# Kernel tuning notes

Measured on AMD Instinct MI355X. Metric: run time of the kernel, lower is better.

Reference implementation:

```python
import jax, jax.numpy as jnp
import numpy as np

D_MODEL = 1024
NUM_HEADS = 16
D_K = D_MODEL // NUM_HEADS
ROPE_THETA = 10000.0


def apply_rope(x, pos):
    # x: [B, H, S, d_k], pos: [S] int
    half = x.shape[-1] // 2
    inv_freq = ROPE_THETA ** (-jnp.arange(half, dtype=jnp.float32) * 2.0 / x.shape[-1])
    ang = pos.astype(jnp.float32)[:, None] * inv_freq[None, :]  # [S, half]
    cos, sin = jnp.cos(ang), jnp.sin(ang)
    x1 = x[..., 0::2]
    x2 = x[..., 1::2]
    r1 = x1 * cos - x2 * sin
    r2 = x1 * sin + x2 * cos
    return jnp.stack([r1, r2], axis=-1).reshape(x.shape)


def setup_inputs() -> dict:
    key = jax.random.key(0)
    ks = jax.random.split(key, 5)
    B, S = 4, 2048
    scale = 1.0 / np.sqrt(D_MODEL)
    x = jax.random.normal(ks[0], (B, S, D_MODEL), dtype=jnp.float32)
    w_q = jax.random.normal(ks[1], (D_MODEL, D_MODEL), dtype=jnp.float32) * scale
    w_k = jax.random.normal(ks[2], (D_MODEL, D_MODEL), dtype=jnp.float32) * scale
    w_v = jax.random.normal(ks[3], (D_MODEL, D_MODEL), dtype=jnp.float32) * scale
    w_o = jax.random.normal(ks[4], (D_MODEL, D_MODEL), dtype=jnp.float32) * scale
    token_positions = jnp.arange(S, dtype=jnp.int32)
    return {"x": x, "w_q": w_q, "w_k": w_k, "w_v": w_v, "w_o": w_o, "token_positions": token_positions}


def reference(x, w_q, w_k, w_v, w_o, token_positions):
    B, S, _ = x.shape
    def proj(w):
        return (x @ w.T).reshape(B, S, NUM_HEADS, D_K).transpose(0, 2, 1, 3)  # [B,H,S,d_k]
    q, k, v = proj(w_q), proj(w_k), proj(w_v)
    q = apply_rope(q, token_positions)
    k = apply_rope(k, token_positions)
    logits = jnp.einsum('bhid,bhjd->bhij', q, k) / jnp.sqrt(jnp.float32(D_K))
    causal = jnp.tril(jnp.ones((S, S), dtype=bool))
    logits = jnp.where(causal[None, None], logits, -jnp.inf)
    weights = jax.nn.softmax(logits, axis=-1)
    attn = jnp.einsum('bhij,bhjd->bhid', weights, v)  # [B,H,S,d_k]
    attn = attn.transpose(0, 2, 1, 3).reshape(B, S, D_MODEL)
    return attn @ w_o.T
```

## Files before the change

### kernel.cpp

```cpp
#include <hip/hip_runtime.h>
#include <hip/hip_bf16.h>
#include <stdint.h>

#define DM   1024
#define SEQ  2048
#define BATCH 4
#define NH   16
#define DK   64
#define NTK  16

typedef __attribute__((ext_vector_type(8))) __bf16 bf16x8;
typedef __attribute__((ext_vector_type(4))) float f32x4;
typedef __attribute__((ext_vector_type(4))) unsigned short ushort4_t;
typedef __attribute__((ext_vector_type(4))) unsigned int uint4_t;

typedef __attribute__((address_space(1))) const unsigned int GU32;
typedef __attribute__((address_space(3))) unsigned int LU32;

__device__ inline void gl_lds16(const void* g, void* l) {
  __builtin_amdgcn_global_load_lds((GU32*)g, (LU32*)l, 16, 0, 0);
}

__device__ inline f32x4 mfma16(bf16x8 a, bf16x8 b, f32x4 c) {
  return __builtin_amdgcn_mfma_f32_16x16x32_bf16(a, b, c, 0, 0, 0);
}

__device__ inline unsigned short f2bf(float f) {
  unsigned u = __float_as_uint(f);
  u += 0x7fffu + ((u >> 16) & 1u);
  return (unsigned short)(u >> 16);
}

__device__ inline unsigned cvt_pk_bf16(float a, float b) {
  unsigned r;
  asm("v_cvt_pk_bf16_f32 %0, %1, %2" : "=v"(r) : "v"(a), "v"(b));
  return r;
}

__device__ inline float fexp2(float x) {
  float r;
  asm("v_exp_f32 %0, %1" : "=v"(r) : "v"(x));
  return r;
}

__device__ inline float fmax3(float a, float b, float c) {
  float r;
  asm("v_max3_f32 %0, %1, %2, %3" : "=v"(r) : "v"(a), "v"(b), "v"(c));
  return r;
}

__device__ inline int swz_of(int r) { return ((r & 6) << 2) | ((r & 1) << 5); }
__device__ inline int bswz(int r) { return ((r & 6) << 3) | ((r & 1) << 6); }

__global__ void prep_kernel(const float* __restrict__ x,
                            const float* __restrict__ wq, const float* __restrict__ wk,
                            const float* __restrict__ wv, const float* __restrict__ wo,
                            const int* __restrict__ tp,
                            unsigned short* __restrict__ xbf,
                            unsigned short* __restrict__ wbf,
                            float2* __restrict__ tab)
{
  const int NX4 = (BATCH*SEQ*DM)/4;
  const int NW4 = (DM*DM)/4;
  int idx = blockIdx.x*256 + threadIdx.x;
  if (idx < NX4) {
    float4 v = ((const float4*)x)[idx];
    ushort4_t o; o[0]=f2bf(v.x); o[1]=f2bf(v.y); o[2]=f2bf(v.z); o[3]=f2bf(v.w);
    ((ushort4_t*)xbf)[idx] = o;
  } else if (idx < NX4 + 4*NW4) {
    int t = idx - NX4;
    int wsel = t >> 18;
    int off = t & (NW4-1);
    const float* src = (wsel==0) ? wq : (wsel==1) ? wk : (wsel==2) ? wv : wo;
    float4 v = ((const float4*)src)[off];
    ushort4_t o; o[0]=f2bf(v.x); o[1]=f2bf(v.y); o[2]=f2bf(v.z); o[3]=f2bf(v.w);
    ((ushort4_t*)wbf)[wsel*NW4 + off] = o;
  } else {
    int t = idx - NX4 - 4*NW4;
    if (t < SEQ*32) {
      int s = t >> 5, i = t & 31;
      float invf = exp2f(-(float)i * (13.287712379549449f/32.0f));
      float ang = (float)tp[s] * invf;
      float sn, cs; sincosf(ang, &sn, &cs);
      tab[t] = make_float2(cs, sn);
    }
  }
}

template<int MODE>
__global__ __launch_bounds__(256, 2)
void gemm_db(const unsigned short* __restrict__ A,
             const unsigned short* __restrict__ Wall,
             unsigned short* __restrict__ qbf,
             unsigned short* __restrict__ kbf,
             unsigned short* __restrict__ vt,
             float* __restrict__ ofp,
             const float2* __restrict__ tab)
{
  __shared__ __align__(16) char lds[65536];
  const int tid = threadIdx.x;
  const int bid = blockIdx.x;
  int sel, mt, nt;
  if (MODE == 0) {
    sel = bid >> 9;
    int r = bid & 511;
    int xcd = r & 7, idx = r >> 3;
    mt = xcd*8 + (idx >> 3);  nt = idx & 7;
  } else {
    sel = 3;
    int xcd = bid & 7, idx = bid >> 3;
    mt = xcd*8 + (idx >> 3);  nt = idx & 7;
  }
  const unsigned short* Bm = Wall + (size_t)sel*DM*DM;
  const int a0 = mt*128, b0r = nt*128;
  const int w = tid>>6, lane = tid&63, ln = lane&15, g = lane>>4;
  const int wm = (w>>1)*64, wn = (w&1)*64;

  const char* src[8];
  {
    int rr = tid >> 3;
    int c  = (tid & 7) * 8;
    #pragma unroll
    for (int i = 0; i < 4; ++i) {
      int r_ = i*32 + rr;
      int cs = c ^ swz_of(r_);
      src[i]   = (const char*)(A  + (size_t)(a0  + r_)*DM + cs);
      src[i+4] = (const char*)(Bm + (size_t)(b0r + r_)*DM + cs);
    }
  }

  int offA[4], offB[4];
  #pragma unroll
  for (int m = 0; m < 4; ++m) {
    int R  = wm + m*16 + ln;
    offA[m] = R*128 + ((g*8 ^ swz_of(R)) * 2);
    int Rb = wn + m*16 + ln;
    offB[m] = 16384 + Rb*128 + ((g*8 ^ swz_of(Rb)) * 2);
  }

  f32x4 acc[4][4];
  #pragma unroll
  for (int i=0;i<4;i++)
    #pragma unroll
    for (int j=0;j<4;j++) acc[i][j] = (f32x4){0.f,0.f,0.f,0.f};

  #pragma unroll
  for (int i = 0; i < 8; ++i) gl_lds16(src[i],       lds +         i*4096 + tid*16);
  #pragma unroll
  for (int i = 0; i < 8; ++i) gl_lds16(src[i] + 128, lds + 32768 + i*4096 + tid*16);

  for (int t = 0; t < NTK; ++t) {
    char* sb = lds + (t & 1) * 32768;
    if (t < NTK-1) asm volatile("s_waitcnt vmcnt(8)" ::: "memory");
    else           asm volatile("s_waitcnt vmcnt(0)" ::: "memory");
    __builtin_amdgcn_sched_barrier(0);
    __builtin_amdgcn_s_barrier();
    asm volatile("" ::: "memory");
    __builtin_amdgcn_sched_barrier(0);

    bf16x8 fa[4][2], fb[4][2];
    #pragma unroll
    for (int m = 0; m < 4; ++m) {
      fa[m][0] = *(const bf16x8*)(sb + offA[m]);
      fa[m][1] = *(const bf16x8*)(sb + (offA[m] ^ 64));
      fb[m][0] = *(const bf16x8*)(sb + offB[m]);
      fb[m][1] = *(const bf16x8*)(sb + (offB[m] ^ 64));
    }
    asm volatile("s_waitcnt lgkmcnt(0)" ::: "memory");
    __builtin_amdgcn_sched_barrier(0);
    __builtin_amdgcn_s_barrier();
    asm volatile("" ::: "memory");
    __builtin_amdgcn_sched_barrier(0);

    if (t + 2 < NTK) {
      const int kb = (t + 2) * 128;
      #pragma unroll
      for (int i = 0; i < 8; ++i)
        gl_lds16(src[i] + kb, sb + i*4096 + tid*16);
    }
    __builtin_amdgcn_s_setprio(1);
    #pragma unroll
    for (int h = 0; h < 2; ++h)
      #pragma unroll
      for (int m = 0; m < 4; ++m)
        #pragma unroll
        for (int n = 0; n < 4; ++n)
          acc[m][n] = mfma16(fa[m][h], fb[n][h], acc[m][n]);
    __builtin_amdgcn_s_setprio(0);
  }

  if (MODE == 1) {
    #pragma unroll
    for (int i=0;i<4;i++) {
      int m = a0 + wm + i*16 + g*4;
      #pragma unroll
      for (int jn=0;jn<4;jn++) {
        int n = b0r + wn + jn*16 + ln;
        #pragma unroll
        for (int j=0;j<4;j++)
          ofp[(size_t)(m+j)*DM + n] = acc[i][jn][j];
      }
    }
  } else if (sel == 2) {
    #pragma unroll
    for (int i=0;i<4;i++) {
      int m0 = a0 + wm + i*16 + g*4;
      int bb = m0>>11, s0 = m0&2047;
      #pragma unroll
      for (int jn=0;jn<4;jn++) {
        int n = b0r + wn + jn*16 + ln;
        int h = n>>6, d = n&63;
        ushort4_t o4;
        #pragma unroll
        for (int j=0;j<4;j++) o4[j] = f2bf(acc[i][jn][j]);
        *(ushort4_t*)&vt[(((size_t)bb*NH + h)*DK + d)*SEQ + s0] = o4;
      }
    }
  } else {
    unsigned short* dst = sel ? kbf : qbf;
    const float qs = sel ? 1.0f : 0.1803368802f;
    #pragma unroll
    for (int jn=0;jn<4;jn++) {
      int n = b0r + wn + jn*16 + ln;
      int h = n>>6, d = n&63, di = d>>1, par = d&1;
      #pragma unroll
      for (int i=0;i<4;i++) {
        #pragma unroll
        for (int j=0;j<4;j++) {
          int m = a0 + wm + i*16 + g*4 + j;
          int bb = m>>11, s = m&2047;
          float v = acc[i][jn][j];
          float pv = __shfl_xor(v, 1);
          float2 cssn = tab[s*32 + di];
          float r = par ? (v*cssn.x + pv*cssn.y) : (v*cssn.x - pv*cssn.y);
          dst[((size_t)(bb*NH + h)*SEQ + s)*DK + d] = f2bf(r*qs);
        }
      }
    }
  }
}

__global__ __launch_bounds__(256, 2)
void attn_fa(const unsigned short* __restrict__ qbf,
             const unsigned short* __restrict__ kbf,
             const unsigned short* __restrict__ vtg,
             unsigned short* __restrict__ attnbf)
{
  __shared__ __align__(16) char kv_lds[32768];
  __shared__ unsigned short PlA[4][16][72];
  __shared__ unsigned short PlB[4][16][72];
  const int bh = blockIdx.x, qblk = 15 - blockIdx.y;
  const int tid = threadIdx.x, w = tid>>6, lane = tid&63, ln = lane&15, g = lane>>4;
  const int q0a = qblk*128 + w*16;
  const int q0b = q0a + 64;
  const int NT = 2*qblk + 2;

  const unsigned short* qrowA = qbf + ((size_t)bh*SEQ + q0a + ln)*DK;
  const unsigned short* qrowB = qbf + ((size_t)bh*SEQ + q0b + ln)*DK;
  bf16x8 qa0 = *(const bf16x8*)(qrowA + g*8);
  bf16x8 qa1 = *(const bf16x8*)(qrowA + 32 + g*8);
  bf16x8 qb0 = *(const bf16x8*)(qrowB + g*8);
  bf16x8 qb1 = *(const bf16x8*)(qrowB + 32 + g*8);

  uint4_t ov = {0x3F803F80u, 0x3F803F80u, 0x3F803F80u, 0x3F803F80u};
  const bf16x8 ones = *(bf16x8*)&ov;

  const int rr = tid >> 3;
  const int cb = (tid & 7) * 16;
  const char* ks0 = (const char*)(kbf + ((size_t)bh*SEQ + rr     )*DK) + (cb ^ bswz(rr));
  const char* ks1 = (const char*)(kbf + ((size_t)bh*SEQ + rr + 32)*DK) + (cb ^ bswz(rr));
  const char* vs0 = (const char*)(vtg + ((size_t)bh*DK  + rr     )*SEQ) + (cb ^ bswz(rr));
  const char* vs1 = (const char*)(vtg + ((size_t)bh*DK  + rr + 32)*SEQ) + (cb ^ bswz(rr));

  const int ok0 = (g*16) ^ bswz(ln);

  gl_lds16(ks0, kv_lds +         tid*16);
  gl_lds16(ks1, kv_lds +  4096 + tid*16);
  gl_lds16(vs0, kv_lds +  8192 + tid*16);
  gl_lds16(vs1, kv_lds + 12288 + tid*16);
  gl_lds16(ks0 + 8192, kv_lds + 16384 +         tid*16);
  gl_lds16(ks1 + 8192, kv_lds + 16384 +  4096 + tid*16);
  gl_lds16(vs0 + 128,  kv_lds + 16384 +  8192 + tid*16);
  gl_lds16(vs1 + 128,  kv_lds + 16384 + 12288 + tid*16);

  f32x4 oA[4], oB[4], osA, osB;
  #pragma unroll
  for (int f=0;f<4;f++) { oA[f] = (f32x4){0,0,0,0}; oB[f] = (f32x4){0,0,0,0}; }
  osA = (f32x4){0,0,0,0}; osB = (f32x4){0,0,0,0};
  float mA = -1e30f, mB = -1e30f;
  const int qgA = q0a + ln, qgB = q0b + ln;

  for (int t = 0; t < NT; ++t) {
    char* sb = kv_lds + (t & 1) * 16384;
    if (t < NT-1) asm volatile("s_waitcnt vmcnt(4)" ::: "memory");
    else          asm volatile("s_waitcnt vmcnt(0)" ::: "memory");
    __builtin_amdgcn_sched_barrier(0);
    __builtin_amdgcn_s_barrier();
    asm volatile("" ::: "memory");
    __builtin_amdgcn_sched_barrier(0);

    bf16x8 kf[4][2], vfr[4][2];
    #pragma unroll
    for (int a=0;a<4;a++) {
      kf[a][0]  = *(const bf16x8*)(sb + a*2048 + (ok0 ^  0) + ln*128);
      kf[a][1]  = *(const bf16x8*)(sb + a*2048 + (ok0 ^ 64) + ln*128);
      vfr[a][0] = *(const bf16x8*)(sb + 8192 + a*2048 + (ok0 ^  0) + ln*128);
      vfr[a][1] = *(const bf16x8*)(sb + 8192 + a*2048 + (ok0 ^ 64) + ln*128);
    }
    asm volatile("s_waitcnt lgkmcnt(0)" ::: "memory");
    __builtin_amdgcn_sched_barrier(0);
    __builtin_amdgcn_s_barrier();
    asm volatile("" ::: "memory");
    __builtin_amdgcn_sched_barrier(0);

    if (t + 2 < NT) {
      const size_t kO = (size_t)(t+2)*8192, vO = (size_t)(t+2)*128;
      gl_lds16(ks0 + kO, sb +         tid*16);
      gl_lds16(ks1 + kO, sb +  4096 + tid*16);
      gl_lds16(vs0 + vO, sb +  8192 + tid*16);
      gl_lds16(vs1 + vO, sb + 12288 + tid*16);
    }

    const bool actA = (t < NT-1);

    f32x4 saA[4], saB[4];
    __builtin_amdgcn_s_setprio(1);
    #pragma unroll
    for (int kvf=0;kvf<4;kvf++) {
      f32x4 zb = (f32x4){0,0,0,0};
      zb = mfma16(kf[kvf][0], qb0, zb);
      zb = mfma16(kf[kvf][1], qb1, zb);
      saB[kvf] = zb;
    }
    if (actA) {
      #pragma unroll
      for (int kvf=0;kvf<4;kvf++) {
        f32x4 za = (f32x4){0,0,0,0};
        za = mfma16(kf[kvf][0], qa0, za);
        za = mfma16(kf[kvf][1], qa1, za);
        saA[kvf] = za;
      }
    }
    __builtin_amdgcn_s_setprio(0);

    if (actA) {
      if (t == NT-2) {
        int thr = qgA - t*64 - g*4;
        #pragma unroll
        for (int kvf=0;kvf<4;kvf++)
          #pragma unroll
          for (int j=0;j<4;j++)
            if (kvf*16 + j > thr) saA[kvf][j] = -1e30f;
      }
      float lm = fmax3(saA[0][0], saA[0][1], saA[0][2]);
      lm = fmax3(lm, saA[0][3], saA[1][0]);
      lm = fmax3(lm, saA[1][1], saA[1][2]);
      lm = fmax3(lm, saA[1][3], saA[2][0]);
      lm = fmax3(lm, saA[2][1], saA[2][2]);
      lm = fmax3(lm, saA[2][3], saA[3][0]);
      lm = fmax3(lm, saA[3][1], saA[3][2]);
      lm = fmaxf(lm, saA[3][3]);
      lm = fmaxf(lm, __shfl_xor(lm, 16));
      lm = fmaxf(lm, __shfl_xor(lm, 32));
      if (!__all(lm - mA <= 8.0f)) {
        float mnew = fmaxf(mA, lm);
        float corr = fexp2(mA - mnew);
        #pragma unroll
        for (int j=0;j<4;j++) {
          float cj = __shfl(corr, g*4 + j);
          #pragma unroll
          for (int f=0;f<4;f++) oA[f][j] *= cj;
          osA[j] *= cj;
        }
        mA = mnew;
      }
      #pragma unroll
      for (int kvf=0;kvf<4;kvf++) {
        float p0 = fexp2(saA[kvf][0] - mA);
        float p1 = fexp2(saA[kvf][1] - mA);
        float p2 = fexp2(saA[kvf][2] - mA);
        float p3 = fexp2(saA[kvf][3] - mA);
        uint2 pk;
        pk.x = cvt_pk_bf16(p0, p1);
        pk.y = cvt_pk_bf16(p2, p3);
        *(uint2*)&PlA[w][ln][kvf*16 + g*4] = pk;
      }
    }

    {
      if (t == NT-1) {
        int thr = qgB - t*64 - g*4;
        #pragma unroll
        for (int kvf=0;kvf<4;kvf++)
          #pragma unroll
          for (int j=0;j<4;j++)
            if (kvf*16 + j > thr) saB[kvf][j] = -1e30f;
      }
      float lm = fmax3(saB[0][0], saB[0][1], saB[0][2]);
      lm = fmax3(lm, saB[0][3], saB[1][0]);
      lm = fmax3(lm, saB[1][1], saB[1][2]);
      lm = fmax3(lm, saB[1][3], saB[2][0]);
      lm = fmax3(lm, saB[2][1], saB[2][2]);
      lm = fmax3(lm, saB[2][3], saB[3][0]);
      lm = fmax3(lm, saB[3][1], saB[3][2]);
      lm = fmaxf(lm, saB[3][3]);
      lm = fmaxf(lm, __shfl_xor(lm, 16));
      lm = fmaxf(lm, __shfl_xor(lm, 32));
      if (!__all(lm - mB <= 8.0f)) {
        float mnew = fmaxf(mB, lm);
        float corr = fexp2(mB - mnew);
        #pragma unroll
        for (int j=0;j<4;j++) {
          float cj = __shfl(corr, g*4 + j);
          #pragma unroll
          for (int f=0;f<4;f++) oB[f][j] *= cj;
          osB[j] *= cj;
        }
        mB = mnew;
      }
      #pragma unroll
      for (int kvf=0;kvf<4;kvf++) {
        float p0 = fexp2(saB[kvf][0] - mB);
        float p1 = fexp2(saB[kvf][1] - mB);
        float p2 = fexp2(saB[kvf][2] - mB);
        float p3 = fexp2(saB[kvf][3] - mB);
        uint2 pk;
        pk.x = cvt_pk_bf16(p0, p1);
        pk.y = cvt_pk_bf16(p2, p3);
        *(uint2*)&PlB[w][ln][kvf*16 + g*4] = pk;
      }
    }

    asm volatile("s_waitcnt lgkmcnt(0)" ::: "memory");

    __builtin_amdgcn_s_setprio(1);
    #pragma unroll
    for (int c=0;c<2;c++) {
      bf16x8 pfB = *(const bf16x8*)&PlB[w][ln][c*32 + g*8];
      #pragma unroll
      for (int f=0;f<4;f++)
        oB[f] = mfma16(pfB, vfr[f][c], oB[f]);
      osB = mfma16(pfB, ones, osB);
    }
    if (actA) {
      #pragma unroll
      for (int c=0;c<2;c++) {
        bf16x8 pfA = *(const bf16x8*)&PlA[w][ln][c*32 + g*8];
        #pragma unroll
        for (int f=0;f<4;f++)
          oA[f] = mfma16(pfA, vfr[f][c], oA[f]);
        osA = mfma16(pfA, ones, osA);
      }
    }
    __builtin_amdgcn_s_setprio(0);
  }

  const int bb = bh>>4, h = bh&15;
  #pragma unroll
  for (int j=0;j<4;j++) {
    float liA = 1.0f / osA[j];
    float liB = 1.0f / osB[j];
    int sA = q0a + g*4 + j, sB = q0b + g*4 + j;
    #pragma unroll
    for (int f=0;f<4;f++) {
      attnbf[((size_t)bb*SEQ + sA)*DM + h*DK + f*16 + ln] = f2bf(oA[f][j]*liA);
      attnbf[((size_t)bb*SEQ + sB)*DM + h*DK + f*16 + ln] = f2bf(oB[f][j]*liB);
    }
  }
}

extern "C" void kernel_launch(void* const* d_in, const int* in_sizes, int n_in,
                              void* d_out, int out_size, void* d_ws, size_t ws_size,
                              hipStream_t stream)
{
  const float* x  = (const float*)d_in[0];
  const float* wq = (const float*)d_in[1];
  const float* wk = (const float*)d_in[2];
  const float* wv = (const float*)d_in[3];
  const float* wo = (const float*)d_in[4];
  const int*   tp = (const int*)d_in[5];

  const size_t XB = (size_t)BATCH*SEQ*DM*2;
  const size_t WB = (size_t)DM*DM*2;

  char* ws = (char*)d_ws;
  unsigned short* xbf = (unsigned short*)(ws);
  unsigned short* qbf = (unsigned short*)(ws + XB);
  unsigned short* kbf = (unsigned short*)(ws + 2*XB);
  unsigned short* vt  = (unsigned short*)(ws + 3*XB);
  unsigned short* abf = (unsigned short*)(ws + 4*XB);
  unsigned short* wbf = (unsigned short*)(ws + 5*XB);
  float2* tab = (float2*)(ws + 5*XB + 4*WB);

  prep_kernel<<<12544, 256, 0, stream>>>(x, wq, wk, wv, wo, tp, xbf, wbf, tab);

  gemm_db<0><<<1536, 256, 0, stream>>>(xbf, wbf, qbf, kbf, vt, nullptr, tab);
  attn_fa<<<dim3(64,16), 256, 0, stream>>>(qbf, kbf, vt, abf);
  gemm_db<1><<<512, 256, 0, stream>>>(abf, wbf, nullptr, nullptr, nullptr,
                                      (float*)d_out, nullptr);
}
```

Baseline: 176.0 us.

## Pair complementary causal query blocks per workgroup to balance attention work

Each attention workgroup now handles two query blocks, qh=15-by and by, processing their KV tiles back to back in one continuous double-buffered loop of 34 tiles. The grid is halved to 64x8. Every block gets the same causal workload, which removes tail imbalance and lets the KV prefetch pipeline run across the boundary between the two query blocks. The trade-off is fewer workgroups, which reduces occupancy slack. It also adds a mid-loop epilogue that writes the first block's output and reloads Q.

```diff
diff --git a/kernel.cpp b/kernel.cpp
--- a/kernel.cpp
+++ b/kernel.cpp
@@ -249,18 +249,12 @@
   __shared__ __align__(16) char kv_lds[32768];
   __shared__ unsigned short PlA[4][16][72];
   __shared__ unsigned short PlB[4][16][72];
-  const int bh = blockIdx.x, qblk = 15 - blockIdx.y;
+  const int bh = blockIdx.x, by = blockIdx.y;
+  const int qh = 15 - by;
+  const int NTa = 2*qh + 2;
+  const int NTtot = 34;
   const int tid = threadIdx.x, w = tid>>6, lane = tid&63, ln = lane&15, g = lane>>4;
-  const int q0a = qblk*128 + w*16;
-  const int q0b = q0a + 64;
-  const int NT = 2*qblk + 2;
-
-  const unsigned short* qrowA = qbf + ((size_t)bh*SEQ + q0a + ln)*DK;
-  const unsigned short* qrowB = qbf + ((size_t)bh*SEQ + q0b + ln)*DK;
-  bf16x8 qa0 = *(const bf16x8*)(qrowA + g*8);
-  bf16x8 qa1 = *(const bf16x8*)(qrowA + 32 + g*8);
-  bf16x8 qb0 = *(const bf16x8*)(qrowB + g*8);
-  bf16x8 qb1 = *(const bf16x8*)(qrowB + 32 + g*8);
+  const int bb = bh>>4, h = bh&15;
 
   uint4_t ov = {0x3F803F80u, 0x3F803F80u, 0x3F803F80u, 0x3F803F80u};
   const bf16x8 ones = *(bf16x8*)&ov;
@@ -283,17 +277,27 @@
   gl_lds16(vs0 + 128,  kv_lds + 16384 +  8192 + tid*16);
   gl_lds16(vs1 + 128,  kv_lds + 16384 + 12288 + tid*16);
 
+  int q0a = qh*128 + w*16;
+  int q0b = q0a + 64;
+  const unsigned short* qrowA = qbf + ((size_t)bh*SEQ + q0a + ln)*DK;
+  const unsigned short* qrowB = qbf + ((size_t)bh*SEQ + q0b + ln)*DK;
+  bf16x8 qa0 = *(const bf16x8*)(qrowA + g*8);
+  bf16x8 qa1 = *(const bf16x8*)(qrowA + 32 + g*8);
+  bf16x8 qb0 = *(const bf16x8*)(qrowB + g*8);
+  bf16x8 qb1 = *(const bf16x8*)(qrowB + 32 + g*8);
+
   f32x4 oA[4], oB[4], osA, osB;
   #pragma unroll
   for (int f=0;f<4;f++) { oA[f] = (f32x4){0,0,0,0}; oB[f] = (f32x4){0,0,0,0}; }
   osA = (f32x4){0,0,0,0}; osB = (f32x4){0,0,0,0};
   float mA = -1e30f, mB = -1e30f;
-  const int qgA = q0a + ln, qgB = q0b + ln;
-
-  for (int t = 0; t < NT; ++t) {
-    char* sb = kv_lds + (t & 1) * 16384;
-    if (t < NT-1) asm volatile("s_waitcnt vmcnt(4)" ::: "memory");
-    else          asm volatile("s_waitcnt vmcnt(0)" ::: "memory");
+
+  for (int u = 0; u < NTtot; ++u) {
+    const int tloc  = (u < NTa) ? u : u - NTa;
+    const int NTcur = (u < NTa) ? NTa : NTtot - NTa;
+    char* sb = kv_lds + (u & 1) * 16384;
+    if (u < NTtot-1) asm volatile("s_waitcnt vmcnt(4)" ::: "memory");
+    else             asm volatile("s_waitcnt vmcnt(0)" ::: "memory");
     __builtin_amdgcn_sched_barrier(0);
     __builtin_amdgcn_s_barrier();
     asm volatile("" ::: "memory");
@@ -313,15 +317,42 @@
     asm volatile("" ::: "memory");
     __builtin_amdgcn_sched_barrier(0);
 
-    if (t + 2 < NT) {
-      const size_t kO = (size_t)(t+2)*8192, vO = (size_t)(t+2)*128;
+    if (u + 2 < NTtot) {
+      const int t2 = (u + 2 < NTa) ? u + 2 : u + 2 - NTa;
+      const size_t kO = (size_t)t2*8192, vO = (size_t)t2*128;
       gl_lds16(ks0 + kO, sb +         tid*16);
       gl_lds16(ks1 + kO, sb +  4096 + tid*16);
       gl_lds16(vs0 + vO, sb +  8192 + tid*16);
       gl_lds16(vs1 + vO, sb + 12288 + tid*16);
     }
 
-    const bool actA = (t < NT-1);
+    if (u == NTa) {
+      #pragma unroll
+      for (int j=0;j<4;j++) {
+        float liA = 1.0f / osA[j];
+        float liB = 1.0f / osB[j];
+        int sA = q0a + g*4 + j, sB = q0b + g*4 + j;
+        #pragma unroll
+        for (int f=0;f<4;f++) {
+          attnbf[((size_t)bb*SEQ + sA)*DM + h*DK + f*16 + ln] = f2bf(oA[f][j]*liA);
+          attnbf[((size_t)bb*SEQ + sB)*DM + h*DK + f*16 + ln] = f2bf(oB[f][j]*liB);
+        }
+      }
+      q0a = by*128 + w*16;
+      q0b = q0a + 64;
+      const unsigned short* qrA = qbf + ((size_t)bh*SEQ + q0a + ln)*DK;
+      const unsigned short* qrB = qbf + ((size_t)bh*SEQ + q0b + ln)*DK;
+      qa0 = *(const bf16x8*)(qrA + g*8);
+      qa1 = *(const bf16x8*)(qrA + 32 + g*8);
+      qb0 = *(const bf16x8*)(qrB + g*8);
+      qb1 = *(const bf16x8*)(qrB + 32 + g*8);
+      #pragma unroll
+      for (int f=0;f<4;f++) { oA[f] = (f32x4){0,0,0,0}; oB[f] = (f32x4){0,0,0,0}; }
+      osA = (f32x4){0,0,0,0}; osB = (f32x4){0,0,0,0};
+      mA = -1e30f; mB = -1e30f;
+    }
+
+    const bool actA = (tloc < NTcur-1);
 
     f32x4 saA[4], saB[4];
     __builtin_amdgcn_s_setprio(1);
@@ -344,8 +375,8 @@
     __builtin_amdgcn_s_setprio(0);
 
     if (actA) {
-      if (t == NT-2) {
-        int thr = qgA - t*64 - g*4;
+      if (tloc == NTcur-2) {
+        int thr = q0a + ln - tloc*64 - g*4;
         #pragma unroll
         for (int kvf=0;kvf<4;kvf++)
           #pragma unroll
@@ -388,8 +419,8 @@
     }
 
     {
-      if (t == NT-1) {
-        int thr = qgB - t*64 - g*4;
+      if (tloc == NTcur-1) {
+        int thr = q0b + ln - tloc*64 - g*4;
         #pragma unroll
         for (int kvf=0;kvf<4;kvf++)
           #pragma unroll
@@ -455,7 +486,6 @@
     __builtin_amdgcn_s_setprio(0);
   }
 
-  const int bb = bh>>4, h = bh&15;
   #pragma unroll
   for (int j=0;j<4;j++) {
     float liA = 1.0f / osA[j];
@@ -495,7 +525,7 @@
   prep_kernel<<<12544, 256, 0, stream>>>(x, wq, wk, wv, wo, tp, xbf, wbf, tab);
 
   gemm_db<0><<<1536, 256, 0, stream>>>(xbf, wbf, qbf, kbf, vt, nullptr, tab);
-  attn_fa<<<dim3(64,16), 256, 0, stream>>>(qbf, kbf, vt, abf);
+  attn_fa<<<dim3(64,8), 256, 0, stream>>>(qbf, kbf, vt, abf);
   gemm_db<1><<<512, 256, 0, stream>>>(abf, wbf, nullptr, nullptr, nullptr,
                                       (float*)d_out, nullptr);
 }
```

After: 174.8 us. About the same (-0.7%).
